# Kernel optimization log

Measured on AMD Instinct MI355X. Metric: run time of the kernel, lower is better.

Reference implementation:

```python
import jax, jax.numpy as jnp
import numpy as np

T_DATA = 20000
E_NO = 2000
I_NO = 500
SUB = 12
T_SYN = 200
T_HIST = 100
SB = 3   # syn_basis_no
HB = 3   # hist_basis_no
PB = 3   # prop_basis_no


def setup_inputs() -> dict:
    key = jax.random.key(0)
    ks = jax.random.split(key, 20)
    f32 = jnp.float32
    S_e = (jax.random.uniform(ks[0], (T_DATA, E_NO)) < 0.05).astype(f32)
    S_i = (jax.random.uniform(ks[1], (T_DATA, I_NO)) < 0.05).astype(f32)
    C_syn_e = (jax.random.uniform(ks[2], (SUB, E_NO)) < 1.0 / SUB).astype(f32)
    C_syn_i = (jax.random.uniform(ks[3], (SUB, I_NO)) < 1.0 / SUB).astype(f32)
    # dendritic adjacency: strictly lower-triangular-ish sparse connectivity
    C_den = (jax.random.uniform(ks[4], (SUB, SUB)) < 0.15).astype(f32) * jnp.tril(jnp.ones((SUB, SUB), f32), -1)
    return {
        'S_e': S_e, 'S_i': S_i,
        'C_syn_e': C_syn_e, 'C_syn_i': C_syn_i, 'C_den': C_den,
        'W_s_syn': jax.random.normal(ks[5], (SUB, SB, 2), f32) * 0.04,
        'W_ns_syn': jax.random.normal(ks[6], (SUB, SB, 2), f32) * 0.02,
        'Delta_s_syn': jax.random.uniform(ks[7], (SUB, 2), f32),
        'Delta_ns_syn': jax.random.uniform(ks[8], (SUB, 2), f32),
        'Theta_s': jnp.zeros((SUB,), f32),
        'Theta_ns': jnp.zeros((SUB,), f32),
        'W_s_sub': jax.random.uniform(ks[9], (SUB,), f32),
        'W_ns_sub': jax.random.uniform(ks[10], (SUB,), f32),
        'W_s_hist': jax.random.uniform(ks[11], (SUB - 1, HB), f32) * -0.04,
        'W_ns_hist': jax.random.uniform(ks[12], (SUB - 1, HB), f32) * -0.02,
        'W_s_prop': jax.random.uniform(ks[13], (SUB, PB), f32) * 0.04,
        'W_ns_prop': jax.random.uniform(ks[14], (SUB, PB), f32) * 0.02,
    }


def _syn_kernels(W, Delta):
    # W: [sub, SB, 2], Delta: [sub, 2] -> kern [sub, 2, T_SYN]
    t = jnp.arange(T_SYN, dtype=jnp.float32)
    ts = jnp.maximum(t[None, None, :] - jnp.exp(Delta)[:, :, None], 0.0)  # [sub,2,T]
    tau = jnp.exp(jnp.arange(SB, dtype=jnp.float32) * 0.5)                # Tau = arange(0, SB*0.5, 0.5)
    tt = ts[:, None, :, :] / tau[None, :, None, None]                     # [sub,SB,2,T]
    return jnp.einsum('sbct,sbc->sct', tt * jnp.exp(-tt), W)


def _decay_kernels(W, T, nb):
    # W: [n, nb] -> kern [n, T]; tau_b = exp(0.5*b)
    t = jnp.arange(T, dtype=jnp.float32)
    tau = jnp.exp(jnp.arange(nb, dtype=jnp.float32) * 0.5)
    tt = t[None, :] / tau[:, None]  # [nb, T]
    return jnp.einsum('bt,sb->st', tt * jnp.exp(-tt), W)


def _causal_conv(x, kern):
    # x: [T, C], kern: [C, K]; out[t, c] = sum_k kern[c, k] * x[t-k, c]
    C, K = kern.shape
    y = jax.lax.conv_general_dilated(
        x.T[None], kern[:, None, ::-1], (1,), [(K - 1, 0)],
        feature_group_count=C, dimension_numbers=('NCW', 'OIW', 'NCW'))
    return y[0].T


def reference(S_e, S_i, C_syn_e, C_syn_i, C_den, W_s_syn, W_ns_syn,
              Delta_s_syn, Delta_ns_syn, Theta_s, Theta_ns,
              W_s_sub, W_ns_sub, W_s_hist, W_ns_hist, W_s_prop, W_ns_prop):
    sub = C_den.shape[0]
    # --- synaptic kernels + causal filtering (vectorized over subunits) ---
    k_s = _syn_kernels(W_s_syn, Delta_s_syn)      # [sub,2,T_SYN]
    k_ns = _syn_kernels(W_ns_syn, Delta_ns_syn)
    IN_e = S_e @ C_syn_e.T                        # [T, sub]
    IN_i = S_i @ C_syn_i.T
    syn_s_in = _causal_conv(IN_e, k_s[:, 0]) + _causal_conv(IN_i, k_s[:, 1])    # [T, sub]
    syn_ns_in = _causal_conv(IN_e, k_ns[:, 0]) + _causal_conv(IN_i, k_ns[:, 1])
    # --- history / propagation kernels ---
    hist_s = _decay_kernels(W_s_hist, T_HIST, HB)   # [sub-1, T_HIST]
    hist_ns = _decay_kernels(W_ns_hist, T_HIST, HB)
    prop_s = _decay_kernels(W_s_prop, T_HIST, PB)   # [sub, T_HIST]
    prop_ns = _decay_kernels(W_ns_prop, T_HIST, PB)
    # Z_pad (spike history buffer) stays zero in this forward, so the filtered
    # hist/prop terms are identically zero; keep the computation for fidelity.
    z0 = jnp.zeros((sub - 1, T_HIST), syn_s_in.dtype)
    filt_s_hist = (hist_s * z0).sum(-1)      # [sub-1]
    filt_ns_hist = (hist_ns * z0).sum(-1)
    sp0 = C_den[:, 1:] @ z0                   # [sub, T_HIST]
    filt_s_prop = (prop_s * sp0).sum(-1)      # [sub]
    filt_ns_prop = (prop_ns * sp0).sum(-1)

    def step(carry, syn_t):
        Y_s, Y_ns = carry
        s_t, ns_t = syn_t
        X_s = s_t + filt_s_prop + C_den @ Y_s + Theta_s
        X_s = X_s.at[1:].add(filt_s_hist)
        X_ns = ns_t + filt_ns_prop + C_den @ Y_ns + Theta_ns
        X_ns = X_ns.at[1:].add(filt_ns_hist)
        X_ns_out = jax.nn.sigmoid(X_ns)
        Y_ns_n = X_ns_out * W_ns_sub
        sig_s = jax.nn.sigmoid(X_s)
        Y_s_n = jnp.concatenate([sig_s[:1] * W_s_sub[:1], X_ns_out[1:] * W_s_sub[1:]])
        # per-step output: [Y_s(t+1), Y_ns(t+1), spike probs of non-root subunits]
        return (Y_s_n, Y_ns_n), jnp.concatenate([Y_s_n, Y_ns_n, sig_s[1:]])

    init = (jnp.zeros((sub,), syn_s_in.dtype), jnp.zeros((sub,), syn_s_in.dtype))
    _, out = jax.lax.scan(step, init, (syn_s_in, syn_ns_in))
    return out  # [T_DATA, 3*sub - 1]


if __name__ == '__main__':
    inp = setup_inputs()
    o = reference(**inp)
    print(o.shape)
```

## Files before the change

### kernel.cpp

```cpp
#include <hip/hip_runtime.h>

typedef unsigned int uint;
typedef unsigned long long u64;

#define TD 20000
#define WS_H      0
#define WS_SPREAD 9600
#define WS_IN     14600
#define WS_SYN    494600

__device__ __forceinline__ float sigf(float x) { return 1.f / (1.f + __expf(-x)); }

__global__ __launch_bounds__(256) void k1_precomp(
    const float* __restrict__ Ce, const float* __restrict__ Ci,
    const float* __restrict__ Wsy_s, const float* __restrict__ Wsy_ns,
    const float* __restrict__ Del_s, const float* __restrict__ Del_ns,
    float* __restrict__ ws) {
  int p = blockIdx.x * 256 + threadIdx.x;
  if (p < 2400) {
    int k = p / 12, s = p - (p / 12) * 12;
    float o[4];
    for (int ch = 0; ch < 2; ++ch) {
      const float* W = ch ? Wsy_ns : Wsy_s;
      const float* D = ch ? Del_ns : Del_s;
      for (int c = 0; c < 2; ++c) {
        float ts = fmaxf((float)k - __expf(D[s * 2 + c]), 0.f);
        float v = 0.f;
        for (int b = 0; b < 3; ++b) {
          float tt = ts * __expf(-0.5f * (float)b);
          v += W[s * 6 + b * 2 + c] * tt * __expf(-tt);
        }
        o[ch * 2 + c] = v;
      }
    }
    float* H = ws + WS_H + (size_t)(k * 12 + s) * 4;
    H[0] = o[0]; H[1] = o[1]; H[2] = o[2]; H[3] = o[3];
  }
  int q = p - 2400;
  if (q >= 0 && q < 2500) {
    uint m = 0;
    if (q < 2000) {
      for (int s = 0; s < 12; ++s) m |= (Ce[s * 2000 + q] != 0.f ? (1u << s) : 0u);
    } else {
      int e = q - 2000;
      for (int s = 0; s < 12; ++s) m |= (Ci[s * 500 + e] != 0.f ? (1u << s) : 0u);
    }
    u64 sp = 0ull;
    for (int s = 0; s < 12; ++s) sp |= (u64)((m >> s) & 1u) << (5 * s);
    ((uint2*)(ws + WS_SPREAD))[q] = make_uint2((uint)sp, (uint)(sp >> 32));
  }
}

__global__ __launch_bounds__(256) void k2_project(
    const float* __restrict__ Se, const float* __restrict__ Si,
    float* __restrict__ ws) {
  __shared__ __align__(16) uint2 sp[2520];
  {
    const uint2* g = (const uint2*)(ws + WS_SPREAD);
    for (int p = threadIdx.x; p < 2500; p += 256) sp[p] = g[p];
    if (threadIdx.x < 20) sp[2500 + threadIdx.x] = make_uint2(0u, 0u);
  }
  __syncthreads();
  const int lane = threadIdx.x & 63;
  const int t = blockIdx.x * 4 + (threadIdx.x >> 6);
  const uint4* SP4 = (const uint4*)sp;
  float* INb = ws + WS_IN;

  const float4 z4 = make_float4(0.f, 0.f, 0.f, 0.f);
  const float4* Sr = (const float4*)(Se + (size_t)t * 2000);
  const float4* Sir = (const float4*)(Si + (size_t)t * 500);
  float4 sv[8];
#pragma unroll
  for (int it = 0; it < 7; ++it) sv[it] = Sr[lane + it * 64];
  sv[7] = (lane < 52) ? Sr[448 + lane] : z4;
  float4 si0 = Sir[lane];
  float4 si1 = (lane < 61) ? Sir[64 + lane] : z4;

  uint eTot[12];
#pragma unroll
  for (int s = 0; s < 12; ++s) eTot[s] = 0u;
  u64 acc = 0ull;
#pragma unroll
  for (int it = 0; it < 8; ++it) {
    int i4 = lane + it * 64;
    uint4 a = SP4[2 * i4];
    uint4 b = SP4[2 * i4 + 1];
    u64 m0 = (u64)a.x | ((u64)a.y << 32);
    u64 m1 = (u64)a.z | ((u64)a.w << 32);
    u64 m2 = (u64)b.x | ((u64)b.y << 32);
    u64 m3 = (u64)b.z | ((u64)b.w << 32);
    acc += (sv[it].x != 0.f ? m0 : 0ull);
    acc += (sv[it].y != 0.f ? m1 : 0ull);
    acc += (sv[it].z != 0.f ? m2 : 0ull);
    acc += (sv[it].w != 0.f ? m3 : 0ull);
    if (it == 3) {
#pragma unroll
      for (int s = 0; s < 12; ++s) eTot[s] += (uint)(acc >> (5 * s)) & 31u;
      acc = 0ull;
    }
  }
#pragma unroll
  for (int s = 0; s < 12; ++s) eTot[s] += (uint)(acc >> (5 * s)) & 31u;

  u64 accI = 0ull;
  {
    int i4 = lane;
    uint4 a = SP4[1000 + 2 * i4];
    uint4 b = SP4[1000 + 2 * i4 + 1];
    accI += (si0.x != 0.f ? ((u64)a.x | ((u64)a.y << 32)) : 0ull);
    accI += (si0.y != 0.f ? ((u64)a.z | ((u64)a.w << 32)) : 0ull);
    accI += (si0.z != 0.f ? ((u64)b.x | ((u64)b.y << 32)) : 0ull);
    accI += (si0.w != 0.f ? ((u64)b.z | ((u64)b.w << 32)) : 0ull);
    i4 = 64 + lane;
    uint4 c = SP4[1000 + 2 * i4];
    uint4 d = SP4[1000 + 2 * i4 + 1];
    accI += (si1.x != 0.f ? ((u64)c.x | ((u64)c.y << 32)) : 0ull);
    accI += (si1.y != 0.f ? ((u64)c.z | ((u64)c.w << 32)) : 0ull);
    accI += (si1.z != 0.f ? ((u64)d.x | ((u64)d.y << 32)) : 0ull);
    accI += (si1.w != 0.f ? ((u64)d.z | ((u64)d.w << 32)) : 0ull);
  }

  uint pk[12];
#pragma unroll
  for (int s = 0; s < 12; ++s)
    pk[s] = eTot[s] | (((uint)(accI >> (5 * s)) & 31u) << 16);
#pragma unroll
  for (int s = 0; s < 12; ++s) {
    uint v = pk[s];
    v += __shfl_xor(v, 32, 64);
    v += __shfl_xor(v, 16, 64);
    v += __shfl_xor(v, 8, 64);
    v += __shfl_xor(v, 4, 64);
    v += __shfl_xor(v, 2, 64);
    v += __shfl_xor(v, 1, 64);
    pk[s] = v;
  }
  if (lane == 0) {
    float4* o = (float4*)(INb + (size_t)t * 24);
    o[0] = make_float4((float)(pk[0] & 0xffffu), (float)(pk[1] & 0xffffu),
                       (float)(pk[2] & 0xffffu), (float)(pk[3] & 0xffffu));
    o[1] = make_float4((float)(pk[4] & 0xffffu), (float)(pk[5] & 0xffffu),
                       (float)(pk[6] & 0xffffu), (float)(pk[7] & 0xffffu));
    o[2] = make_float4((float)(pk[8] & 0xffffu), (float)(pk[9] & 0xffffu),
                       (float)(pk[10] & 0xffffu), (float)(pk[11] & 0xffffu));
    o[3] = make_float4((float)(pk[0] >> 16), (float)(pk[1] >> 16),
                       (float)(pk[2] >> 16), (float)(pk[3] >> 16));
    o[4] = make_float4((float)(pk[4] >> 16), (float)(pk[5] >> 16),
                       (float)(pk[6] >> 16), (float)(pk[7] >> 16));
    o[5] = make_float4((float)(pk[8] >> 16), (float)(pk[9] >> 16),
                       (float)(pk[10] >> 16), (float)(pk[11] >> 16));
  }
}

__global__ __launch_bounds__(256) void k3_conv(float* __restrict__ ws) {
  __shared__ float tile[6 * 264];
  __shared__ float red[4 * 64 * 7];
  const int g = blockIdx.y;
  const int t0 = blockIdx.x * 64;
  const float* INb = ws + WS_IN;
  for (int p = threadIdx.x; p < 263 * 6; p += 256) {
    int row = p / 6, c = p - row * 6;
    int ch = (c < 3) ? (3 * g + c) : (9 + 3 * g + c);
    int gt = t0 - 199 + row;
    tile[c * 264 + row] = (gt >= 0 && gt < TD) ? INb[(size_t)gt * 24 + ch] : 0.f;
  }
  __syncthreads();
  const int lane = threadIdx.x & 63;
  const int q = threadIdx.x >> 6;
  const float4* H4 = (const float4*)(ws + WS_H);
  float accs[3] = {0.f, 0.f, 0.f}, accn[3] = {0.f, 0.f, 0.f};
  for (int kk = 0; kk < 25; ++kk) {
    int k = q * 50 + kk * 2;
    int rb = lane + 198 - k;
#pragma unroll
    for (int s = 0; s < 3; ++s) {
      float ve0 = tile[s * 264 + rb];
      float ve1 = tile[s * 264 + rb + 1];
      float vi0 = tile[(3 + s) * 264 + rb];
      float vi1 = tile[(3 + s) * 264 + rb + 1];
      float4 h0 = H4[k * 12 + 3 * g + s];
      float4 h1 = H4[(k + 1) * 12 + 3 * g + s];
      accs[s] += h0.x * ve1 + h0.y * vi1 + h1.x * ve0 + h1.y * vi0;
      accn[s] += h0.z * ve1 + h0.w * vi1 + h1.z * ve0 + h1.w * vi0;
    }
  }
  float* mr = red + (q * 64 + lane) * 7;
#pragma unroll
  for (int s = 0; s < 3; ++s) { mr[s] = accs[s]; mr[3 + s] = accn[s]; }
  __syncthreads();
  for (int p = threadIdx.x; p < 64 * 6; p += 256) {
    int row = p / 6, c = p - row * 6;
    if (t0 + row < TD) {
      float sum = red[row * 7 + c] + red[(64 + row) * 7 + c] +
                  red[(128 + row) * 7 + c] + red[(192 + row) * 7 + c];
      int ch = (c < 3) ? (3 * g + c) : (9 + 3 * g + c);
      ws[WS_SYN + (size_t)(t0 + row) * 24 + ch] = sum;
    }
  }
}

__global__ void k45_out(
    const float* __restrict__ Cden, const float* __restrict__ Ws_sub,
    const float* __restrict__ Wns_sub, const float* __restrict__ Th_s,
    const float* __restrict__ Th_ns, const float* __restrict__ ws,
    float* __restrict__ out) {
  __shared__ float lout[64 * 35];
  const int t = blockIdx.x * 64 + threadIdx.x;
  float v[35];
#pragma unroll
  for (int m = 0; m < 35; ++m) v[m] = 0.f;
  if (t < TD) {
    const float* SYN = ws + WS_SYN;
    float dns[12][12];
#pragma unroll
    for (int i = 1; i < 12; ++i)
#pragma unroll
      for (int j = 0; j < i; ++j) dns[i][j] = Cden[i * 12 + j] * Wns_sub[j];
    float th[12];
#pragma unroll
    for (int i = 0; i < 12; ++i) th[i] = Th_ns[i];
    float ap[12], an[12];
#pragma unroll
    for (int i = 0; i < 12; ++i) { ap[i] = 0.f; an[i] = 0.f; }
    int start = t - 12; if (start < 0) start = 0;
    for (int tau = start; tau <= t; ++tau) {
      const float4* sr = (const float4*)(SYN + (size_t)tau * 24 + 12);
      float4 s0 = sr[0], s1 = sr[1], s2 = sr[2];
      float sn[12] = {s0.x, s0.y, s0.z, s0.w, s1.x, s1.y, s1.z, s1.w,
                      s2.x, s2.y, s2.z, s2.w};
#pragma unroll
      for (int i = 0; i < 12; ++i) {
        float x = sn[i] + th[i];
#pragma unroll
        for (int j = 0; j < i; ++j) x += dns[i][j] * ap[j];
        an[i] = sigf(x);
      }
      if (tau < t) {
#pragma unroll
        for (int i = 0; i < 12; ++i) ap[i] = an[i];
      }
    }
    float sns[12];
    {
      const float4* sr = (const float4*)(SYN + (size_t)t * 24);
      float4 s0 = sr[0], s1 = sr[1], s2 = sr[2];
      sns[0] = s0.x; sns[1] = s0.y; sns[2] = s0.z; sns[3] = s0.w;
      sns[4] = s1.x; sns[5] = s1.y; sns[6] = s1.z; sns[7] = s1.w;
      sns[8] = s2.x; sns[9] = s2.y; sns[10] = s2.z; sns[11] = s2.w;
    }
    float carry[12];
    carry[0] = (t > 0) ? Ws_sub[0] * sigf(SYN[(size_t)(t - 1) * 24] + Th_s[0]) : 0.f;
#pragma unroll
    for (int j = 1; j < 12; ++j) carry[j] = Ws_sub[j] * ap[j];
    float B[12];
#pragma unroll
    for (int i = 0; i < 12; ++i) {
      float x = sns[i] + Th_s[i];
#pragma unroll
      for (int j = 0; j < i; ++j) x += Cden[i * 12 + j] * carry[j];
      B[i] = sigf(x);
    }
    v[0] = B[0] * Ws_sub[0];
#pragma unroll
    for (int i = 1; i < 12; ++i) v[i] = an[i] * Ws_sub[i];
#pragma unroll
    for (int i = 0; i < 12; ++i) v[12 + i] = an[i] * Wns_sub[i];
#pragma unroll
    for (int i = 1; i < 12; ++i) v[23 + i] = B[i];
  }
#pragma unroll
  for (int m = 0; m < 35; ++m) lout[threadIdx.x * 35 + m] = v[m];
  __syncthreads();
  const int t0 = blockIdx.x * 64;
  int nrow = TD - t0; if (nrow > 64) nrow = 64;
  const int valid = nrow * 35;
  for (int p = threadIdx.x; p < valid; p += 64) out[(size_t)t0 * 35 + p] = lout[p];
}

extern "C" void kernel_launch(void* const* d_in, const int* in_sizes, int n_in,
                              void* d_out, int out_size, void* d_ws, size_t ws_size,
                              hipStream_t stream) {
  const float* Se = (const float*)d_in[0];
  const float* Si = (const float*)d_in[1];
  const float* Ce = (const float*)d_in[2];
  const float* Ci = (const float*)d_in[3];
  const float* Cden = (const float*)d_in[4];
  const float* Wsy_s = (const float*)d_in[5];
  const float* Wsy_ns = (const float*)d_in[6];
  const float* Del_s = (const float*)d_in[7];
  const float* Del_ns = (const float*)d_in[8];
  const float* Th_s = (const float*)d_in[9];
  const float* Th_ns = (const float*)d_in[10];
  const float* Ws_sub = (const float*)d_in[11];
  const float* Wns_sub = (const float*)d_in[12];
  float* ws = (float*)d_ws;
  float* out = (float*)d_out;

  k1_precomp<<<20, 256, 0, stream>>>(Ce, Ci, Wsy_s, Wsy_ns, Del_s, Del_ns, ws);
  k2_project<<<5000, 256, 0, stream>>>(Se, Si, ws);
  dim3 g3(313, 4);
  k3_conv<<<g3, 256, 0, stream>>>(ws);
  k45_out<<<313, 64, 0, stream>>>(Cden, Ws_sub, Wns_sub, Th_s, Th_ns, ws, out);
}
```

Before: 330.3 us.

## Use a persistent grid and a bank-conflict-free LDS mask layout in projection

The precompute kernel now stores the spread connectivity masks split by index modulo 4 (four planes of 512/128 entries), with the zero padding written explicitly. The projection kernel reads these as strided uint2 so that lanes touch consecutive LDS words instead of 16-byte pairs, which is meant to cut bank conflicts. The projection kernel also becomes grid-stride, launching 2048 blocks with occupancy hint 8, so each block loads the 20 KB mask table once and reuses it across several timesteps. The risk is a tail imbalance: 20000 rows over 8192 waves is not an even split.

```diff
diff --git a/kernel.cpp b/kernel.cpp
--- a/kernel.cpp
+++ b/kernel.cpp
@@ -4,10 +4,11 @@
 typedef unsigned long long u64;
 
 #define TD 20000
-#define WS_H      0
-#define WS_SPREAD 9600
-#define WS_IN     14600
-#define WS_SYN    494600
+#define WS_H   0
+#define WS_ME  9600
+#define WS_MI  13696
+#define WS_IN  14720
+#define WS_SYN 494720
 
 __device__ __forceinline__ float sigf(float x) { return 1.f / (1.f + __expf(-x)); }
 
@@ -47,108 +48,128 @@
     }
     u64 sp = 0ull;
     for (int s = 0; s < 12; ++s) sp |= (u64)((m >> s) & 1u) << (5 * s);
-    ((uint2*)(ws + WS_SPREAD))[q] = make_uint2((uint)sp, (uint)(sp >> 32));
-  }
-}
-
-__global__ __launch_bounds__(256) void k2_project(
+    uint2 v = make_uint2((uint)sp, (uint)(sp >> 32));
+    if (q < 2000) {
+      int g = q >> 2, j = q & 3;
+      ((uint2*)(ws + WS_ME))[j * 512 + g] = v;
+    } else {
+      int e = q - 2000;
+      int g = e >> 2, j = e & 3;
+      ((uint2*)(ws + WS_MI))[j * 128 + g] = v;
+    }
+  }
+  int z = p - 4900;
+  if (z >= 0 && z < 48) {
+    int j = z / 12, g = 500 + z % 12;
+    ((uint2*)(ws + WS_ME))[j * 512 + g] = make_uint2(0u, 0u);
+  }
+  int zi = p - 4948;
+  if (zi >= 0 && zi < 12) {
+    int j = zi / 3, g = 125 + zi % 3;
+    ((uint2*)(ws + WS_MI))[j * 128 + g] = make_uint2(0u, 0u);
+  }
+}
+
+__global__ __launch_bounds__(256, 8) void k2_project(
     const float* __restrict__ Se, const float* __restrict__ Si,
     float* __restrict__ ws) {
-  __shared__ __align__(16) uint2 sp[2520];
+  __shared__ __align__(16) uint2 sp[2560];
   {
-    const uint2* g = (const uint2*)(ws + WS_SPREAD);
-    for (int p = threadIdx.x; p < 2500; p += 256) sp[p] = g[p];
-    if (threadIdx.x < 20) sp[2500 + threadIdx.x] = make_uint2(0u, 0u);
+    const uint2* g = (const uint2*)(ws + WS_ME);
+    for (int p = threadIdx.x; p < 2560; p += 256) sp[p] = g[p];
   }
   __syncthreads();
   const int lane = threadIdx.x & 63;
-  const int t = blockIdx.x * 4 + (threadIdx.x >> 6);
-  const uint4* SP4 = (const uint4*)sp;
+  const int wv = blockIdx.x * 4 + (threadIdx.x >> 6);
   float* INb = ws + WS_IN;
-
   const float4 z4 = make_float4(0.f, 0.f, 0.f, 0.f);
-  const float4* Sr = (const float4*)(Se + (size_t)t * 2000);
-  const float4* Sir = (const float4*)(Si + (size_t)t * 500);
-  float4 sv[8];
-#pragma unroll
-  for (int it = 0; it < 7; ++it) sv[it] = Sr[lane + it * 64];
-  sv[7] = (lane < 52) ? Sr[448 + lane] : z4;
-  float4 si0 = Sir[lane];
-  float4 si1 = (lane < 61) ? Sir[64 + lane] : z4;
-
-  uint eTot[12];
-#pragma unroll
-  for (int s = 0; s < 12; ++s) eTot[s] = 0u;
-  u64 acc = 0ull;
-#pragma unroll
-  for (int it = 0; it < 8; ++it) {
-    int i4 = lane + it * 64;
-    uint4 a = SP4[2 * i4];
-    uint4 b = SP4[2 * i4 + 1];
-    u64 m0 = (u64)a.x | ((u64)a.y << 32);
-    u64 m1 = (u64)a.z | ((u64)a.w << 32);
-    u64 m2 = (u64)b.x | ((u64)b.y << 32);
-    u64 m3 = (u64)b.z | ((u64)b.w << 32);
-    acc += (sv[it].x != 0.f ? m0 : 0ull);
-    acc += (sv[it].y != 0.f ? m1 : 0ull);
-    acc += (sv[it].z != 0.f ? m2 : 0ull);
-    acc += (sv[it].w != 0.f ? m3 : 0ull);
-    if (it == 3) {
-#pragma unroll
-      for (int s = 0; s < 12; ++s) eTot[s] += (uint)(acc >> (5 * s)) & 31u;
-      acc = 0ull;
-    }
-  }
-#pragma unroll
-  for (int s = 0; s < 12; ++s) eTot[s] += (uint)(acc >> (5 * s)) & 31u;
-
-  u64 accI = 0ull;
-  {
-    int i4 = lane;
-    uint4 a = SP4[1000 + 2 * i4];
-    uint4 b = SP4[1000 + 2 * i4 + 1];
-    accI += (si0.x != 0.f ? ((u64)a.x | ((u64)a.y << 32)) : 0ull);
-    accI += (si0.y != 0.f ? ((u64)a.z | ((u64)a.w << 32)) : 0ull);
-    accI += (si0.z != 0.f ? ((u64)b.x | ((u64)b.y << 32)) : 0ull);
-    accI += (si0.w != 0.f ? ((u64)b.z | ((u64)b.w << 32)) : 0ull);
-    i4 = 64 + lane;
-    uint4 c = SP4[1000 + 2 * i4];
-    uint4 d = SP4[1000 + 2 * i4 + 1];
-    accI += (si1.x != 0.f ? ((u64)c.x | ((u64)c.y << 32)) : 0ull);
-    accI += (si1.y != 0.f ? ((u64)c.z | ((u64)c.w << 32)) : 0ull);
-    accI += (si1.z != 0.f ? ((u64)d.x | ((u64)d.y << 32)) : 0ull);
-    accI += (si1.w != 0.f ? ((u64)d.z | ((u64)d.w << 32)) : 0ull);
-  }
-
-  uint pk[12];
-#pragma unroll
-  for (int s = 0; s < 12; ++s)
-    pk[s] = eTot[s] | (((uint)(accI >> (5 * s)) & 31u) << 16);
-#pragma unroll
-  for (int s = 0; s < 12; ++s) {
-    uint v = pk[s];
-    v += __shfl_xor(v, 32, 64);
-    v += __shfl_xor(v, 16, 64);
-    v += __shfl_xor(v, 8, 64);
-    v += __shfl_xor(v, 4, 64);
-    v += __shfl_xor(v, 2, 64);
-    v += __shfl_xor(v, 1, 64);
-    pk[s] = v;
-  }
-  if (lane == 0) {
-    float4* o = (float4*)(INb + (size_t)t * 24);
-    o[0] = make_float4((float)(pk[0] & 0xffffu), (float)(pk[1] & 0xffffu),
-                       (float)(pk[2] & 0xffffu), (float)(pk[3] & 0xffffu));
-    o[1] = make_float4((float)(pk[4] & 0xffffu), (float)(pk[5] & 0xffffu),
-                       (float)(pk[6] & 0xffffu), (float)(pk[7] & 0xffffu));
-    o[2] = make_float4((float)(pk[8] & 0xffffu), (float)(pk[9] & 0xffffu),
-                       (float)(pk[10] & 0xffffu), (float)(pk[11] & 0xffffu));
-    o[3] = make_float4((float)(pk[0] >> 16), (float)(pk[1] >> 16),
-                       (float)(pk[2] >> 16), (float)(pk[3] >> 16));
-    o[4] = make_float4((float)(pk[4] >> 16), (float)(pk[5] >> 16),
-                       (float)(pk[6] >> 16), (float)(pk[7] >> 16));
-    o[5] = make_float4((float)(pk[8] >> 16), (float)(pk[9] >> 16),
-                       (float)(pk[10] >> 16), (float)(pk[11] >> 16));
+
+  for (int t = wv; t < TD; t += 8192) {
+    const float4* Sr = (const float4*)(Se + (size_t)t * 2000);
+    const float4* Sir = (const float4*)(Si + (size_t)t * 500);
+    float4 sv[8];
+#pragma unroll
+    for (int it = 0; it < 7; ++it) sv[it] = Sr[lane + it * 64];
+    sv[7] = (lane < 52) ? Sr[448 + lane] : z4;
+    float4 si0 = Sir[lane];
+    float4 si1 = (lane < 61) ? Sir[64 + lane] : z4;
+
+    uint eTot[12];
+#pragma unroll
+    for (int s = 0; s < 12; ++s) eTot[s] = 0u;
+    u64 acc = 0ull;
+#pragma unroll
+    for (int it = 0; it < 8; ++it) {
+      int i4 = lane + it * 64;
+      uint2 a0 = sp[i4];
+      uint2 a1 = sp[512 + i4];
+      uint2 a2 = sp[1024 + i4];
+      uint2 a3 = sp[1536 + i4];
+      acc += (sv[it].x != 0.f ? ((u64)a0.x | ((u64)a0.y << 32)) : 0ull);
+      acc += (sv[it].y != 0.f ? ((u64)a1.x | ((u64)a1.y << 32)) : 0ull);
+      acc += (sv[it].z != 0.f ? ((u64)a2.x | ((u64)a2.y << 32)) : 0ull);
+      acc += (sv[it].w != 0.f ? ((u64)a3.x | ((u64)a3.y << 32)) : 0ull);
+      if (it == 3) {
+#pragma unroll
+        for (int s = 0; s < 12; ++s) eTot[s] += (uint)(acc >> (5 * s)) & 31u;
+        acc = 0ull;
+      }
+    }
+#pragma unroll
+    for (int s = 0; s < 12; ++s) eTot[s] += (uint)(acc >> (5 * s)) & 31u;
+
+    u64 accI = 0ull;
+    {
+      int i4 = lane;
+      uint2 a0 = sp[2048 + i4];
+      uint2 a1 = sp[2176 + i4];
+      uint2 a2 = sp[2304 + i4];
+      uint2 a3 = sp[2432 + i4];
+      accI += (si0.x != 0.f ? ((u64)a0.x | ((u64)a0.y << 32)) : 0ull);
+      accI += (si0.y != 0.f ? ((u64)a1.x | ((u64)a1.y << 32)) : 0ull);
+      accI += (si0.z != 0.f ? ((u64)a2.x | ((u64)a2.y << 32)) : 0ull);
+      accI += (si0.w != 0.f ? ((u64)a3.x | ((u64)a3.y << 32)) : 0ull);
+      i4 = 64 + lane;
+      uint2 b0 = sp[2048 + i4];
+      uint2 b1 = sp[2176 + i4];
+      uint2 b2 = sp[2304 + i4];
+      uint2 b3 = sp[2432 + i4];
+      accI += (si1.x != 0.f ? ((u64)b0.x | ((u64)b0.y << 32)) : 0ull);
+      accI += (si1.y != 0.f ? ((u64)b1.x | ((u64)b1.y << 32)) : 0ull);
+      accI += (si1.z != 0.f ? ((u64)b2.x | ((u64)b2.y << 32)) : 0ull);
+      accI += (si1.w != 0.f ? ((u64)b3.x | ((u64)b3.y << 32)) : 0ull);
+    }
+
+    uint pk[12];
+#pragma unroll
+    for (int s = 0; s < 12; ++s)
+      pk[s] = eTot[s] | (((uint)(accI >> (5 * s)) & 31u) << 16);
+#pragma unroll
+    for (int s = 0; s < 12; ++s) {
+      uint v = pk[s];
+      v += __shfl_xor(v, 32, 64);
+      v += __shfl_xor(v, 16, 64);
+      v += __shfl_xor(v, 8, 64);
+      v += __shfl_xor(v, 4, 64);
+      v += __shfl_xor(v, 2, 64);
+      v += __shfl_xor(v, 1, 64);
+      pk[s] = v;
+    }
+    if (lane == 0) {
+      float4* o = (float4*)(INb + (size_t)t * 24);
+      o[0] = make_float4((float)(pk[0] & 0xffffu), (float)(pk[1] & 0xffffu),
+                         (float)(pk[2] & 0xffffu), (float)(pk[3] & 0xffffu));
+      o[1] = make_float4((float)(pk[4] & 0xffffu), (float)(pk[5] & 0xffffu),
+                         (float)(pk[6] & 0xffffu), (float)(pk[7] & 0xffffu));
+      o[2] = make_float4((float)(pk[8] & 0xffffu), (float)(pk[9] & 0xffffu),
+                         (float)(pk[10] & 0xffffu), (float)(pk[11] & 0xffffu));
+      o[3] = make_float4((float)(pk[0] >> 16), (float)(pk[1] >> 16),
+                         (float)(pk[2] >> 16), (float)(pk[3] >> 16));
+      o[4] = make_float4((float)(pk[4] >> 16), (float)(pk[5] >> 16),
+                         (float)(pk[6] >> 16), (float)(pk[7] >> 16));
+      o[5] = make_float4((float)(pk[8] >> 16), (float)(pk[9] >> 16),
+                         (float)(pk[10] >> 16), (float)(pk[11] >> 16));
+    }
   }
 }
 
@@ -297,7 +318,7 @@
   float* out = (float*)d_out;
 
   k1_precomp<<<20, 256, 0, stream>>>(Ce, Ci, Wsy_s, Wsy_ns, Del_s, Del_ns, ws);
-  k2_project<<<5000, 256, 0, stream>>>(Se, Si, ws);
+  k2_project<<<2048, 256, 0, stream>>>(Se, Si, ws);
   dim3 g3(313, 4);
   k3_conv<<<g3, 256, 0, stream>>>(ws);
   k45_out<<<313, 64, 0, stream>>>(Cden, Ws_sub, Wns_sub, Th_s, Th_ns, ws, out);
```

Result: slower. 438.0 us (+32.6%).
